# Kernel tuning notes

Hardware: AMD Instinct MI355X
Metric: run time of the kernel (lower is better)

Reference implementation:

```python
import jax, jax.numpy as jnp
import numpy as np

L = 4        # num decoder layers
H = 8        # heads
D = 512      # d_model
DFF = 2048   # ffn hidden
V = 8000     # target vocab
B = 16       # batch
S_ENC = 128  # encoder seq len
T = 32       # decode target_length
START, END, NULL = 1, 2, 0
NEG = -1e9
EPS = 1e-6


def sinusoid_pos(max_len, d):
    pos = np.arange(max_len)[:, None].astype(np.float32)
    i = np.arange(d)[None, :].astype(np.float32)
    ang = pos / np.power(10000.0, (2.0 * np.floor(i / 2.0)) / d)
    pe = np.where(np.arange(d)[None, :] % 2 == 0, np.sin(ang), np.cos(ang))
    return jnp.asarray(pe[None], jnp.float32)  # [1, max_len, d]


def setup_inputs() -> dict:
    key = jax.random.key(0)
    ks = jax.random.split(key, 16)
    g = lambda k, shape: jax.random.normal(k, shape, jnp.float32) * 0.02
    return {
        "target_length": T,
        "encoder_output": jax.random.normal(ks[0], (B, S_ENC, D), jnp.float32),
        "padding_mask": jnp.zeros((B, S_ENC), jnp.float32),  # 1.0 where padded
        "embed": g(ks[1], (V, D)),
        "wq": g(ks[2], (L, D, D)), "wk": g(ks[3], (L, D, D)),
        "wv": g(ks[4], (L, D, D)), "wo": g(ks[5], (L, D, D)),
        "cwq": g(ks[6], (L, D, D)), "cwk": g(ks[7], (L, D, D)),
        "cwv": g(ks[8], (L, D, D)), "cwo": g(ks[9], (L, D, D)),
        "w1": g(ks[10], (L, D, DFF)), "b1": jnp.zeros((L, DFF), jnp.float32),
        "w2": g(ks[11], (L, DFF, D)), "b2": jnp.zeros((L, D), jnp.float32),
        "ln_g": jnp.ones((L, 3, D), jnp.float32), "ln_b": jnp.zeros((L, 3, D), jnp.float32),
        "fc_w": g(ks[12], (D, V)), "fc_b": jnp.zeros((V,), jnp.float32),
    }


def ln(x, g, b):
    m = jnp.mean(x, axis=-1, keepdims=True)
    v = jnp.mean(jnp.square(x - m), axis=-1, keepdims=True)
    return (x - m) * jax.lax.rsqrt(v + EPS) * g + b


def mha(q_in, kv_in, wq, wk, wv, wo, mask):
    Bn, Sq, d = q_in.shape
    dh = d // H
    q = (q_in @ wq).reshape(Bn, Sq, H, dh)
    k = (kv_in @ wk).reshape(Bn, -1, H, dh)
    v = (kv_in @ wv).reshape(Bn, -1, H, dh)
    s = jnp.einsum('bqhd,bkhd->bhqk', q, k) / jnp.sqrt(jnp.float32(dh)) + mask
    a = jax.nn.softmax(s, axis=-1)
    o = jnp.einsum('bhqk,bkhd->bqhd', a, v).reshape(Bn, Sq, d)
    return o @ wo


def decoder_stack(x, encoder_output, self_mask, cross_mask,
                  wq, wk, wv, wo, cwq, cwk, cwv, cwo,
                  w1, b1, w2, b2, ln_g, ln_b):
    for i in range(L):
        a = mha(x, x, wq[i], wk[i], wv[i], wo[i], self_mask)
        x = ln(x + a, ln_g[i, 0], ln_b[i, 0])
        a2 = mha(x, encoder_output, cwq[i], cwk[i], cwv[i], cwo[i], cross_mask)
        x = ln(x + a2, ln_g[i, 1], ln_b[i, 1])
        f = jax.nn.relu(x @ w1[i] + b1[i]) @ w2[i] + b2[i]
        x = ln(x + f, ln_g[i, 2], ln_b[i, 2])
    return x


def reference(target_length, encoder_output, padding_mask, embed,
              wq, wk, wv, wo, cwq, cwk, cwv, cwo,
              w1, b1, w2, b2, ln_g, ln_b, fc_w, fc_b):
    Bn, S, d = encoder_output.shape
    Tp1 = target_length + 1
    pos_enc = sinusoid_pos(Tp1, d)
    sqrt_d = jnp.sqrt(jnp.float32(d))
    cross_mask = padding_mask[:, None, None, :] * NEG  # [B,1,1,S_enc]
    tokens0 = jnp.full((Bn, Tp1), NULL, jnp.int32).at[:, 0].set(START)
    done0 = jnp.zeros((Bn,), bool)

    def step(carry, t):
        tokens, done = carry
        # re-embed the whole (fixed-size, masked) prefix buffer each step
        x = embed[tokens] * sqrt_d + pos_enc
        # only positions <= t are valid keys; no look-ahead mask (matches original)
        self_mask = jnp.where(jnp.arange(Tp1) <= t, 0.0, NEG)[None, None, None, :]
        x = decoder_stack(x, encoder_output, self_mask, cross_mask,
                          wq, wk, wv, wo, cwq, cwk, cwv, cwo,
                          w1, b1, w2, b2, ln_g, ln_b)
        out = x[:, t, :] @ fc_w + fc_b  # logits at last valid position
        max_idx = jnp.argmax(out, axis=-1).astype(jnp.int32)
        done = done | (max_idx == END)
        tok = jnp.where(done, jnp.int32(NULL), max_idx)
        tokens = tokens.at[:, t + 1].set(tok)
        return (tokens, done), None

    (tokens, done), _ = jax.lax.scan(step, (tokens0, done0), jnp.arange(target_length))
    return tokens[:, 1:].astype(jnp.int64)
```

## Files before the change

kernel.cpp:

```cpp
#include <hip/hip_runtime.h>
#include <math.h>

#define L_   4
#define H_   8
#define D_   512
#define DH   64
#define DFF_ 2048
#define V_   8000
#define B_   16
#define SENC 128
#define T_   32
#define TP1  33
#define NEGV -1e9f
#define EPSV 1e-6f
#define SQRTD 22.627416997969522f
#define XSZ  ((size_t)TP1 * B_ * D_)

__global__ __launch_bounds__(256) void gemm32_k(
    const float* __restrict__ A, const float* __restrict__ W,
    const float* __restrict__ bias, float* __restrict__ C,
    int M, int N, int K, int kchunk, size_t pstride, int relu, int tmode)
{
    __shared__ __align__(16) float As[2][16][34];
    __shared__ __align__(16) float Bs[2][16][68];
    int tid = threadIdx.x;
    int tx = tid & 15, ty = tid >> 4;
    int m0 = blockIdx.y * 32, n0 = blockIdx.x * 64;
    int kbeg = blockIdx.z * kchunk;
    int niter = kchunk >> 4;
    C += (size_t)blockIdx.z * pstride;
    int am = tid >> 2, aseg = tid & 3;
    int bk = tid >> 4, bc4 = (tid & 15) * 4;
    float4 aReg = make_float4(0.f, 0.f, 0.f, 0.f), bReg;
    {
        int k0 = kbeg;
        if (tid < 128) {
            int gm = m0 + am;
            if (gm < M) aReg = *(const float4*)&A[(size_t)gm * K + k0 + aseg * 4];
        }
        bReg = *(const float4*)&W[(size_t)(k0 + bk) * N + n0 + bc4];
    }
    if (tid < 128) {
        As[0][aseg * 4 + 0][am] = aReg.x;
        As[0][aseg * 4 + 1][am] = aReg.y;
        As[0][aseg * 4 + 2][am] = aReg.z;
        As[0][aseg * 4 + 3][am] = aReg.w;
    }
    *(float4*)&Bs[0][bk][bc4] = bReg;
    __syncthreads();
    float acc[2][4] = {};
    for (int it = 0; it < niter; it++) {
        int cur = it & 1;
        if (it + 1 < niter) {
            int k0 = kbeg + (it + 1) * 16;
            if (tid < 128) {
                int gm = m0 + am;
                aReg = make_float4(0.f, 0.f, 0.f, 0.f);
                if (gm < M) aReg = *(const float4*)&A[(size_t)gm * K + k0 + aseg * 4];
            }
            bReg = *(const float4*)&W[(size_t)(k0 + bk) * N + n0 + bc4];
        }
        #pragma unroll
        for (int kk = 0; kk < 16; kk++) {
            float2 a2 = *(const float2*)&As[cur][kk][ty * 2];
            float4 b4 = *(const float4*)&Bs[cur][kk][tx * 4];
            acc[0][0] += a2.x * b4.x; acc[0][1] += a2.x * b4.y;
            acc[0][2] += a2.x * b4.z; acc[0][3] += a2.x * b4.w;
            acc[1][0] += a2.y * b4.x; acc[1][1] += a2.y * b4.y;
            acc[1][2] += a2.y * b4.z; acc[1][3] += a2.y * b4.w;
        }
        if (it + 1 < niter) {
            int nxt = 1 - cur;
            if (tid < 128) {
                As[nxt][aseg * 4 + 0][am] = aReg.x;
                As[nxt][aseg * 4 + 1][am] = aReg.y;
                As[nxt][aseg * 4 + 2][am] = aReg.z;
                As[nxt][aseg * 4 + 3][am] = aReg.w;
            }
            *(float4*)&Bs[nxt][bk][bc4] = bReg;
        }
        __syncthreads();
    }
    #pragma unroll
    for (int i = 0; i < 2; i++) {
        int gm = m0 + ty * 2 + i;
        if (gm >= M) continue;
        #pragma unroll
        for (int j = 0; j < 4; j++) {
            int gn = n0 + tx * 4 + j;
            float vv = acc[i][j];
            if (bias) vv += bias[gn];
            if (relu) vv = fmaxf(vv, 0.f);
            if (tmode == 1)
                C[(size_t)(gm >> 7) * 65536 + (size_t)gn * SENC + (gm & 127)] = vv;
            else
                C[(size_t)gm * N + gn] = vv;
        }
    }
}

__global__ __launch_bounds__(256) void gemm_qkv_k(
    const float* __restrict__ A, const float* __restrict__ W0,
    const float* __restrict__ W1, const float* __restrict__ W2,
    float* __restrict__ Cb, int M)
{
    __shared__ __align__(16) float As[2][16][34];
    __shared__ __align__(16) float Bs[2][16][68];
    int sel = blockIdx.x >> 3;
    const float* W = (sel == 0) ? W0 : ((sel == 1) ? W1 : W2);
    float* C = Cb + (size_t)sel * XSZ;
    int tid = threadIdx.x;
    int tx = tid & 15, ty = tid >> 4;
    int m0 = blockIdx.y * 32, n0 = (blockIdx.x & 7) * 64;
    int am = tid >> 2, aseg = tid & 3;
    int bk = tid >> 4, bc4 = (tid & 15) * 4;
    float4 aReg = make_float4(0.f, 0.f, 0.f, 0.f), bReg;
    {
        if (tid < 128) {
            int gm = m0 + am;
            if (gm < M) aReg = *(const float4*)&A[(size_t)gm * D_ + aseg * 4];
        }
        bReg = *(const float4*)&W[(size_t)bk * D_ + n0 + bc4];
    }
    if (tid < 128) {
        As[0][aseg * 4 + 0][am] = aReg.x;
        As[0][aseg * 4 + 1][am] = aReg.y;
        As[0][aseg * 4 + 2][am] = aReg.z;
        As[0][aseg * 4 + 3][am] = aReg.w;
    }
    *(float4*)&Bs[0][bk][bc4] = bReg;
    __syncthreads();
    float acc[2][4] = {};
    for (int it = 0; it < 32; it++) {
        int cur = it & 1;
        if (it + 1 < 32) {
            int k0 = (it + 1) * 16;
            if (tid < 128) {
                int gm = m0 + am;
                aReg = make_float4(0.f, 0.f, 0.f, 0.f);
                if (gm < M) aReg = *(const float4*)&A[(size_t)gm * D_ + k0 + aseg * 4];
            }
            bReg = *(const float4*)&W[(size_t)(k0 + bk) * D_ + n0 + bc4];
        }
        #pragma unroll
        for (int kk = 0; kk < 16; kk++) {
            float2 a2 = *(const float2*)&As[cur][kk][ty * 2];
            float4 b4 = *(const float4*)&Bs[cur][kk][tx * 4];
            acc[0][0] += a2.x * b4.x; acc[0][1] += a2.x * b4.y;
            acc[0][2] += a2.x * b4.z; acc[0][3] += a2.x * b4.w;
            acc[1][0] += a2.y * b4.x; acc[1][1] += a2.y * b4.y;
            acc[1][2] += a2.y * b4.z; acc[1][3] += a2.y * b4.w;
        }
        if (it + 1 < 32) {
            int nxt = 1 - cur;
            if (tid < 128) {
                As[nxt][aseg * 4 + 0][am] = aReg.x;
                As[nxt][aseg * 4 + 1][am] = aReg.y;
                As[nxt][aseg * 4 + 2][am] = aReg.z;
                As[nxt][aseg * 4 + 3][am] = aReg.w;
            }
            *(float4*)&Bs[nxt][bk][bc4] = bReg;
        }
        __syncthreads();
    }
    #pragma unroll
    for (int i = 0; i < 2; i++) {
        int gm = m0 + ty * 2 + i;
        if (gm >= M) continue;
        #pragma unroll
        for (int j = 0; j < 4; j++) {
            int gn = n0 + tx * 4 + j;
            if (sel == 1)
                C[(size_t)(gm & 15) * 16896 + (size_t)gn * TP1 + (gm >> 4)] =
                    acc[i][j];
            else
                C[(size_t)gm * D_ + gn] = acc[i][j];
        }
    }
}

__global__ void init_k(int* __restrict__ tokens, int* __restrict__ done,
                       float* __restrict__ cmask, const float* __restrict__ pm)
{
    int tid = threadIdx.x + blockIdx.x * 256;
    if (tid < B_ * TP1) tokens[tid] = ((tid % TP1) == 0) ? 1 : 0;
    if (tid < B_) done[tid] = 0;
    if (tid < B_ * SENC) cmask[tid] = pm[tid] * NEGV;
}

__global__ __launch_bounds__(256) void embed_k(
    const float* __restrict__ embed, const int* __restrict__ tokens,
    float* __restrict__ x)
{
    int p = blockIdx.x;
    int b = blockIdx.y;
    int tok = tokens[b * TP1 + p];
    const float* e = embed + (size_t)tok * D_;
    float* xr = x + ((size_t)p * B_ + b) * D_;
    for (int d = threadIdx.x; d < D_; d += 256) {
        float fd = (float)(2 * (d / 2)) / (float)D_;
        float ang = (float)p / powf(10000.f, fd);
        float pe = (d & 1) ? cosf(ang) : sinf(ang);
        xr[d] = e[d] * SQRTD + pe;
    }
}

__device__ __forceinline__ float block_sum(float s) {
    __shared__ float red[4];
    #pragma unroll
    for (int off = 32; off; off >>= 1) s += __shfl_xor(s, off);
    if ((threadIdx.x & 63) == 0) red[threadIdx.x >> 6] = s;
    __syncthreads();
    float tot = red[0] + red[1] + red[2] + red[3];
    __syncthreads();
    return tot;
}

__global__ __launch_bounds__(256) void attn_mega_k(
    const float* __restrict__ q, const float* __restrict__ kT,
    const float* __restrict__ v, const float* __restrict__ wo,
    const float* __restrict__ KcT, const float* __restrict__ Vc,
    const float* __restrict__ cmask, const float* __restrict__ cwq,
    const float* __restrict__ cwo, float* __restrict__ x,
    const float* __restrict__ lg, const float* __restrict__ lb, int P)
{
    int r = blockIdx.x, b = r & 15;
    int tid = threadIdx.x;
    int c0 = tid * 2;
    __shared__ float xs[D_], arow[D_];
    __shared__ float scs[H_][SENC];
    __shared__ float inv[H_];
    {
        int kp = tid & 31, h = tid >> 5;
        float acc = 0.f;
        if (kp < P) {
            const float* qr = q + (size_t)r * D_ + h * 64;
            const float* kb = kT + ((size_t)(b * 8 + h) * 64) * TP1 + kp;
            #pragma unroll 8
            for (int d = 0; d < 64; d++) acc += qr[d] * kb[(size_t)d * TP1];
        }
        scs[h][kp] = acc * 0.125f;
    }
    __syncthreads();
    if (tid < 8) {
        float mx = -1e30f;
        for (int j = 0; j < P; j++) mx = fmaxf(mx, scs[tid][j]);
        float sum = 0.f;
        for (int j = 0; j < P; j++) {
            float e = expf(scs[tid][j] - mx);
            scs[tid][j] = e;
            sum += e;
        }
        inv[tid] = 1.f / sum;
    }
    __syncthreads();
    {
        int h = c0 >> 6;
        float o0 = 0.f, o1 = 0.f;
        for (int j = 0; j < P; j++) {
            float2 vv = *(const float2*)&v[((size_t)j * B_ + b) * D_ + c0];
            float w = scs[h][j];
            o0 += w * vv.x; o1 += w * vv.y;
        }
        arow[c0]     = o0 * inv[h];
        arow[c0 + 1] = o1 * inv[h];
    }
    __syncthreads();
    {
        float2 xv = *(const float2*)&x[(size_t)r * D_ + c0];
        float v0 = xv.x, v1 = xv.y;
        #pragma unroll 8
        for (int k = 0; k < D_; k++) {
            float a = arow[k];
            float2 wv = *(const float2*)&wo[(size_t)k * D_ + c0];
            v0 += a * wv.x; v1 += a * wv.y;
        }
        float mean = block_sum(v0 + v1) * (1.f / 512.f);
        float d0 = v0 - mean, d1 = v1 - mean;
        float var = block_sum(d0 * d0 + d1 * d1) * (1.f / 512.f);
        float rs = rsqrtf(var + EPSV);
        xs[c0]     = d0 * rs * lg[c0]     + lb[c0];
        xs[c0 + 1] = d1 * rs * lg[c0 + 1] + lb[c0 + 1];
    }
    __syncthreads();
    {
        float q0 = 0.f, q1 = 0.f;
        #pragma unroll 8
        for (int k = 0; k < D_; k++) {
            float a = xs[k];
            float2 wv = *(const float2*)&cwq[(size_t)k * D_ + c0];
            q0 += a * wv.x; q1 += a * wv.y;
        }
        arow[c0] = q0; arow[c0 + 1] = q1;
    }
    __syncthreads();
    #pragma unroll
    for (int j = 0; j < 4; j++) {
        int idx = tid + j * 256;
        int h = idx >> 7, s = idx & 127;
        const float* kb = KcT + ((size_t)(b * 512 + h * 64)) * SENC + s;
        float acc = 0.f;
        #pragma unroll 8
        for (int d = 0; d < 64; d++) acc += arow[h * 64 + d] * kb[(size_t)d * SENC];
        scs[h][s] = acc * 0.125f + cmask[b * SENC + s];
    }
    __syncthreads();
    if (tid < 8) {
        float mx = -1e30f;
        for (int s = 0; s < SENC; s++) mx = fmaxf(mx, scs[tid][s]);
        float sum = 0.f;
        for (int s = 0; s < SENC; s++) {
            float e = expf(scs[tid][s] - mx);
            scs[tid][s] = e;
            sum += e;
        }
        inv[tid] = 1.f / sum;
    }
    __syncthreads();
    {
        int h = c0 >> 6;
        float o0 = 0.f, o1 = 0.f;
        for (int s = 0; s < SENC; s++) {
            float2 vv = *(const float2*)&Vc[((size_t)b * SENC + s) * D_ + c0];
            float w = scs[h][s];
            o0 += w * vv.x; o1 += w * vv.y;
        }
        arow[c0]     = o0 * inv[h];
        arow[c0 + 1] = o1 * inv[h];
    }
    __syncthreads();
    {
        float v0 = xs[c0], v1 = xs[c0 + 1];
        #pragma unroll 8
        for (int k = 0; k < D_; k++) {
            float a = arow[k];
            float2 wv = *(const float2*)&cwo[(size_t)k * D_ + c0];
            v0 += a * wv.x; v1 += a * wv.y;
        }
        float mean = block_sum(v0 + v1) * (1.f / 512.f);
        float d0 = v0 - mean, d1 = v1 - mean;
        float var = block_sum(d0 * d0 + d1 * d1) * (1.f / 512.f);
        float rs = rsqrtf(var + EPSV);
        x[(size_t)r * D_ + c0]     = d0 * rs * lg[D_ + c0]     + lb[D_ + c0];
        x[(size_t)r * D_ + c0 + 1] = d1 * rs * lg[D_ + c0 + 1] + lb[D_ + c0 + 1];
    }
}

__global__ __launch_bounds__(256) void ln_red_k(
    float* __restrict__ x, const float* __restrict__ parts, size_t pstride,
    int nparts, const float* __restrict__ bias,
    const float* __restrict__ gam, const float* __restrict__ bet)
{
    int r = blockIdx.x;
    float* xr = x + (size_t)r * D_;
    int tid = threadIdx.x;
    float v0 = xr[tid];
    float v1 = xr[tid + 256];
    for (int s = 0; s < nparts; s++) {
        const float* pr = parts + (size_t)s * pstride + (size_t)r * D_;
        v0 += pr[tid];
        v1 += pr[tid + 256];
    }
    if (bias) { v0 += bias[tid]; v1 += bias[tid + 256]; }
    float mean = block_sum(v0 + v1) * (1.f / 512.f);
    float d0 = v0 - mean, d1 = v1 - mean;
    float var = block_sum(d0 * d0 + d1 * d1) * (1.f / 512.f);
    float rs = rsqrtf(var + EPSV);
    xr[tid]       = d0 * rs * gam[tid] + bet[tid];
    xr[tid + 256] = d1 * rs * gam[tid + 256] + bet[tid + 256];
}

__global__ __launch_bounds__(256) void logits_k(
    const float* __restrict__ x, const float* __restrict__ fcw,
    const float* __restrict__ fcb, float* __restrict__ cand_v,
    int* __restrict__ cand_i, int t)
{
    __shared__ float xs[B_][D_];
    __shared__ float red[4][64][B_];
    int tid = threadIdx.x;
    for (int i = tid; i < B_ * D_; i += 256) {
        int b = i >> 9, d = i & 511;
        xs[b][d] = x[((size_t)t * B_ + b) * D_ + d];
    }
    __syncthreads();
    int lane = tid & 63, ks = tid >> 6;
    int col = blockIdx.x * 64 + lane;
    float acc[B_] = {};
    int kb = ks * 128;
    for (int k = kb; k < kb + 128; k++) {
        float w = fcw[(size_t)k * V_ + col];
        #pragma unroll
        for (int b = 0; b < B_; b++) acc[b] += xs[b][k] * w;
    }
    #pragma unroll
    for (int b = 0; b < B_; b++) red[ks][lane][b] = acc[b];
    __syncthreads();
    if (ks == 0) {
        float bias = fcb[col];
        #pragma unroll
        for (int b = 0; b < B_; b++) {
            float val = red[0][lane][b] + red[1][lane][b]
                      + red[2][lane][b] + red[3][lane][b] + bias;
            int idx = col;
            #pragma unroll
            for (int off = 32; off; off >>= 1) {
                float ov = __shfl_down(val, off);
                int oi = __shfl_down(idx, off);
                if (ov > val || (ov == val && oi < idx)) { val = ov; idx = oi; }
            }
            if (lane == 0) {
                cand_v[(size_t)b * 125 + blockIdx.x] = val;
                cand_i[(size_t)b * 125 + blockIdx.x] = idx;
            }
        }
    }
}

__global__ __launch_bounds__(128) void argmax_k(
    const float* __restrict__ cand_v, const int* __restrict__ cand_i,
    int* __restrict__ tokens, int* __restrict__ done, int t)
{
    int b = blockIdx.x;
    int tid = threadIdx.x;
    float val = -1e30f; int idx = 0x7fffffff;
    if (tid < 125) { val = cand_v[(size_t)b * 125 + tid]; idx = cand_i[(size_t)b * 125 + tid]; }
    __shared__ float sv[128];
    __shared__ int si[128];
    sv[tid] = val; si[tid] = idx;
    __syncthreads();
    for (int s = 64; s; s >>= 1) {
        if (tid < s) {
            float ov = sv[tid + s]; int oi = si[tid + s];
            if (ov > sv[tid] || (ov == sv[tid] && oi < si[tid])) {
                sv[tid] = ov; si[tid] = oi;
            }
        }
        __syncthreads();
    }
    if (tid == 0) {
        int best = si[0];
        int dn = done[b] | (best == 2 ? 1 : 0);
        done[b] = dn;
        tokens[b * TP1 + t + 1] = dn ? 0 : best;
    }
}

__global__ void writeout_k(const int* __restrict__ tokens, int* __restrict__ out)
{
    int i = threadIdx.x + blockIdx.x * 256;
    if (i < B_ * T_) {
        int b = i / T_, j = i % T_;
        out[i] = tokens[b * TP1 + j + 1];
    }
}

extern "C" void kernel_launch(void* const* d_in, const int* in_sizes, int n_in,
                              void* d_out, int out_size, void* d_ws, size_t ws_size,
                              hipStream_t stream)
{
    const float* enc   = (const float*)d_in[1];
    const float* pm    = (const float*)d_in[2];
    const float* embed = (const float*)d_in[3];
    const float* wq    = (const float*)d_in[4];
    const float* wk    = (const float*)d_in[5];
    const float* wv    = (const float*)d_in[6];
    const float* wo    = (const float*)d_in[7];
    const float* cwq   = (const float*)d_in[8];
    const float* cwk   = (const float*)d_in[9];
    const float* cwv   = (const float*)d_in[10];
    const float* cwo   = (const float*)d_in[11];
    const float* w1    = (const float*)d_in[12];
    const float* b1    = (const float*)d_in[13];
    const float* w2    = (const float*)d_in[14];
    const float* b2    = (const float*)d_in[15];
    const float* ln_g  = (const float*)d_in[16];
    const float* ln_b  = (const float*)d_in[17];
    const float* fcw   = (const float*)d_in[18];
    const float* fcb   = (const float*)d_in[19];

    float* ws = (float*)d_ws;
    size_t off = 0;
    float* x     = ws + off; off += XSZ;
    float* qkv   = ws + off; off += 3 * XSZ;
    float* parts = ws + off; off += 4 * XSZ;
    float* ffnh  = ws + off; off += (size_t)TP1 * B_ * DFF_;
    float* cand_v= ws + off; off += (size_t)B_ * 125;
    float* KcT   = ws + off; off += (size_t)L_ * B_ * SENC * D_;
    float* Vc    = ws + off; off += (size_t)L_ * B_ * SENC * D_;
    float* cmask = ws + off; off += (size_t)B_ * SENC;
    int* cand_i  = (int*)(ws + off); off += (size_t)B_ * 125;
    int* tokens  = (int*)(ws + off); off += (B_ * TP1 + 63) & ~63;
    int* done    = (int*)(ws + off); off += 64;

    init_k<<<8, 256, 0, stream>>>(tokens, done, cmask, pm);

    const size_t KVL = (size_t)B_ * SENC * D_;
    for (int l = 0; l < L_; l++) {
        gemm32_k<<<dim3(8, (B_ * SENC) / 32), 256, 0, stream>>>(
            enc, cwk + (size_t)l * D_ * D_, nullptr, KcT + l * KVL,
            B_ * SENC, D_, D_, D_, 0, 0, 1);
        gemm32_k<<<dim3(8, (B_ * SENC) / 32), 256, 0, stream>>>(
            enc, cwv + (size_t)l * D_ * D_, nullptr, Vc + l * KVL,
            B_ * SENC, D_, D_, D_, 0, 0, 0);
    }

    for (int t = 0; t < T_; t++) {
        int P = t + 1;
        int M = P * B_;
        int mt = (M + 31) / 32;

        embed_k<<<dim3(P, B_), 256, 0, stream>>>(embed, tokens, x);

        for (int l = 0; l < L_; l++) {
            const size_t lw = (size_t)l * D_ * D_;
            gemm_qkv_k<<<dim3(24, mt), 256, 0, stream>>>(
                x, wq + lw, wk + lw, wv + lw, qkv, M);
            attn_mega_k<<<M, 256, 0, stream>>>(
                qkv, qkv + XSZ, qkv + 2 * XSZ, wo + lw,
                KcT + l * KVL, Vc + l * KVL, cmask, cwq + lw, cwo + lw, x,
                ln_g + (size_t)(l * 3 + 0) * D_, ln_b + (size_t)(l * 3 + 0) * D_, P);
            gemm32_k<<<dim3(32, mt), 256, 0, stream>>>(
                x, w1 + (size_t)l * D_ * DFF_, b1 + (size_t)l * DFF_, ffnh,
                M, DFF_, D_, D_, 0, 1, 0);
            gemm32_k<<<dim3(8, mt, 4), 256, 0, stream>>>(
                ffnh, w2 + (size_t)l * DFF_ * D_, nullptr, parts,
                M, D_, DFF_, 512, XSZ, 0, 0);
            ln_red_k<<<M, 256, 0, stream>>>(x, parts, XSZ, 4, b2 + (size_t)l * D_,
                ln_g + (size_t)(l * 3 + 2) * D_, ln_b + (size_t)(l * 3 + 2) * D_);
        }

        logits_k<<<V_ / 64, 256, 0, stream>>>(x, fcw, fcb, cand_v, cand_i, t);
        argmax_k<<<B_, 128, 0, stream>>>(cand_v, cand_i, tokens, done, t);
    }

    writeout_k<<<2, 256, 0, stream>>>(tokens, (int*)d_out);
}
```

Measured before the change: 24.32 ms.

## Replace per-step kernel launches with a single persistent kernel using grid barriers

Folds all per-step kernels (embedding, QKV GEMM, attention, FFN, logits, argmax, writeout) into one persistent kernel of 256 blocks that steps through work lists and synchronises with an atomic-counter grid barrier. Embeddings of earlier tokens are cached in a separate buffer so each step only embeds the new token, and attention handles four query rows per block. The goal is to remove the launch overhead of hundreds of small kernels across 32 decode steps. The costs are spin-wait barriers, lower per-phase occupancy, and deadlock risk if all 256 blocks are not co-resident.

Measured after the change: 41.23 ms. 1.7x slower.

```diff
diff --git a/kernel.cpp b/kernel.cpp
--- a/kernel.cpp
+++ b/kernel.cpp
@@ -15,31 +15,63 @@
 #define EPSV 1e-6f
 #define SQRTD 22.627416997969522f
 #define XSZ  ((size_t)TP1 * B_ * D_)
-
-__global__ __launch_bounds__(256) void gemm32_k(
+#define KVL  ((size_t)B_ * SENC * D_)
+#define G_   256
+
+struct Prm {
+    const float *enc, *pm, *embed, *wq, *wk, *wv, *wo, *cwq, *cwk, *cwv, *cwo,
+                *w1, *b1, *w2, *b2, *ln_g, *ln_b, *fcw, *fcb;
+    float *x, *xemb, *qkv, *parts, *ffnh, *cand_v, *KcT, *Vc, *cmask;
+    int *cand_i, *tokens, *done, *bar, *outp;
+};
+
+union SMem {
+    struct { float As[2][16][34]; float Bs[2][16][68]; } g;
+    struct { float qa[4][D_]; float xs[4][D_]; float scs[4][H_][SENC];
+             float inv[4][H_]; } a;
+    struct { float xs[B_][D_]; float red[4][64][B_]; } lg;
+    struct { float sv[128]; int si[128]; } am;
+};
+
+__device__ __forceinline__ void gsync(int* cnt, int& epoch) {
+    __syncthreads();
+    if (threadIdx.x == 0) {
+        __threadfence();
+        epoch++;
+        atomicAdd(cnt, 1);
+        while (atomicAdd(cnt, 0) < epoch * G_)
+            __builtin_amdgcn_s_sleep(8);
+        __threadfence();
+    }
+    __syncthreads();
+}
+
+__device__ __forceinline__ float block_sum(float s, float* red) {
+    #pragma unroll
+    for (int off = 32; off; off >>= 1) s += __shfl_xor(s, off);
+    if ((threadIdx.x & 63) == 0) red[threadIdx.x >> 6] = s;
+    __syncthreads();
+    float tot = red[0] + red[1] + red[2] + red[3];
+    __syncthreads();
+    return tot;
+}
+
+__device__ void gemm_tile(float As[2][16][34], float Bs[2][16][68],
     const float* __restrict__ A, const float* __restrict__ W,
     const float* __restrict__ bias, float* __restrict__ C,
-    int M, int N, int K, int kchunk, size_t pstride, int relu, int tmode)
+    int M, int N, int K, int m0, int n0, int kbeg, int niter,
+    int relu, int tmode)
 {
-    __shared__ __align__(16) float As[2][16][34];
-    __shared__ __align__(16) float Bs[2][16][68];
     int tid = threadIdx.x;
     int tx = tid & 15, ty = tid >> 4;
-    int m0 = blockIdx.y * 32, n0 = blockIdx.x * 64;
-    int kbeg = blockIdx.z * kchunk;
-    int niter = kchunk >> 4;
-    C += (size_t)blockIdx.z * pstride;
     int am = tid >> 2, aseg = tid & 3;
     int bk = tid >> 4, bc4 = (tid & 15) * 4;
     float4 aReg = make_float4(0.f, 0.f, 0.f, 0.f), bReg;
-    {
-        int k0 = kbeg;
-        if (tid < 128) {
-            int gm = m0 + am;
-            if (gm < M) aReg = *(const float4*)&A[(size_t)gm * K + k0 + aseg * 4];
-        }
-        bReg = *(const float4*)&W[(size_t)(k0 + bk) * N + n0 + bc4];
-    }
+    if (tid < 128) {
+        int gm = m0 + am;
+        if (gm < M) aReg = *(const float4*)&A[(size_t)gm * K + kbeg + aseg * 4];
+    }
+    bReg = *(const float4*)&W[(size_t)(kbeg + bk) * N + n0 + bc4];
     if (tid < 128) {
         As[0][aseg * 4 + 0][am] = aReg.x;
         As[0][aseg * 4 + 1][am] = aReg.y;
@@ -91,366 +123,432 @@
             float vv = acc[i][j];
             if (bias) vv += bias[gn];
             if (relu) vv = fmaxf(vv, 0.f);
-            if (tmode == 1)
+            if (tmode == 0)
+                C[(size_t)gm * N + gn] = vv;
+            else if (tmode == 1)
                 C[(size_t)(gm >> 7) * 65536 + (size_t)gn * SENC + (gm & 127)] = vv;
             else
-                C[(size_t)gm * N + gn] = vv;
+                C[(size_t)(gm & 15) * 16896 + (size_t)gn * TP1 + (gm >> 4)] = vv;
         }
     }
 }
 
-__global__ __launch_bounds__(256) void gemm_qkv_k(
-    const float* __restrict__ A, const float* __restrict__ W0,
-    const float* __restrict__ W1, const float* __restrict__ W2,
-    float* __restrict__ Cb, int M)
+__global__ __launch_bounds__(256) void decoder_k(Prm p)
 {
-    __shared__ __align__(16) float As[2][16][34];
-    __shared__ __align__(16) float Bs[2][16][68];
-    int sel = blockIdx.x >> 3;
-    const float* W = (sel == 0) ? W0 : ((sel == 1) ? W1 : W2);
-    float* C = Cb + (size_t)sel * XSZ;
-    int tid = threadIdx.x;
-    int tx = tid & 15, ty = tid >> 4;
-    int m0 = blockIdx.y * 32, n0 = (blockIdx.x & 7) * 64;
-    int am = tid >> 2, aseg = tid & 3;
-    int bk = tid >> 4, bc4 = (tid & 15) * 4;
-    float4 aReg = make_float4(0.f, 0.f, 0.f, 0.f), bReg;
-    {
+    extern __shared__ char smem_raw[];
+    SMem& sm = *(SMem*)smem_raw;
+    __shared__ float bsred[4];
+    int bid = blockIdx.x, tid = threadIdx.x;
+    int c0 = tid * 2;
+    int epoch = 0;
+
+    if (bid == 0) {
+        for (int i = tid; i < B_ * TP1; i += 256)
+            p.tokens[i] = ((i % TP1) == 0) ? 1 : 0;
+        if (tid < B_) p.done[tid] = 0;
+    }
+    if (bid == 1) {
+        for (int i = tid; i < B_ * SENC; i += 256)
+            p.cmask[i] = p.pm[i] * NEGV;
+    }
+    gsync(p.bar, epoch);
+
+    for (int job = bid; job < L_ * 1024; job += G_) {
+        int l = job >> 10;
+        int w = job & 1;
+        int jn = (job >> 1) & 7;
+        int mr = (job >> 4) & 63;
+        gemm_tile(sm.g.As, sm.g.Bs, p.enc,
+                  (w ? p.cwv : p.cwk) + (size_t)l * D_ * D_, nullptr,
+                  (w ? p.Vc : p.KcT) + (size_t)l * KVL,
+                  B_ * SENC, D_, D_, mr * 32, jn * 64, 0, 32, 0, w ? 0 : 1);
+    }
+    gsync(p.bar, epoch);
+
+    for (int t = 0; t < T_; t++) {
+        int P = t + 1;
+        int M = P * B_;
+        int mt = (M + 31) / 32;
+
+        for (int job = bid; job < B_; job += G_) {
+            int b = job;
+            if (t > 0) {
+                if (tid < 128) {
+                    sm.am.sv[tid] = (tid < 125) ? p.cand_v[(size_t)b * 125 + tid] : -1e30f;
+                    sm.am.si[tid] = (tid < 125) ? p.cand_i[(size_t)b * 125 + tid] : 0x7fffffff;
+                }
+                __syncthreads();
+                for (int s = 64; s; s >>= 1) {
+                    if (tid < s) {
+                        float ov = sm.am.sv[tid + s]; int oi = sm.am.si[tid + s];
+                        if (ov > sm.am.sv[tid] ||
+                            (ov == sm.am.sv[tid] && oi < sm.am.si[tid])) {
+                            sm.am.sv[tid] = ov; sm.am.si[tid] = oi;
+                        }
+                    }
+                    __syncthreads();
+                }
+                if (tid == 0) {
+                    int idx = sm.am.si[0];
+                    int dn = p.done[b] | (idx == 2 ? 1 : 0);
+                    p.done[b] = dn;
+                    int tok = dn ? 0 : idx;
+                    p.tokens[b * TP1 + t] = tok;
+                    sm.am.si[0] = tok;
+                }
+                __syncthreads();
+            } else {
+                if (tid == 0) sm.am.si[0] = 1;
+                __syncthreads();
+            }
+            int tok = sm.am.si[0];
+            const float* e = p.embed + (size_t)tok * D_;
+            float* xr = p.xemb + ((size_t)t * B_ + b) * D_;
+            #pragma unroll
+            for (int u = 0; u < 2; u++) {
+                int c = c0 + u;
+                float fd = (float)(2 * (c / 2)) / (float)D_;
+                float ang = (float)t / powf(10000.f, fd);
+                float pe = (c & 1) ? cosf(ang) : sinf(ang);
+                xr[c] = e[c] * SQRTD + pe;
+            }
+            __syncthreads();
+        }
+        gsync(p.bar, epoch);
+
+        for (int l = 0; l < L_; l++) {
+            const size_t lw = (size_t)l * D_ * D_;
+            const float* lgam = p.ln_g + (size_t)l * 3 * D_;
+            const float* lbet = p.ln_b + (size_t)l * 3 * D_;
+
+            const float* Aq = (l == 0) ? p.xemb : p.x;
+            int jmod = (l == 0) ? 25 : 24;
+            int nq = jmod * mt;
+            for (int job = bid; job < nq; job += G_) {
+                int jn = job % jmod;
+                int mr = job / jmod;
+                if (jn < 24) {
+                    int sel = jn >> 3;
+                    const float* W = (sel == 0) ? p.wq + lw
+                                   : (sel == 1) ? p.wk + lw : p.wv + lw;
+                    gemm_tile(sm.g.As, sm.g.Bs, Aq, W, nullptr,
+                              p.qkv + (size_t)sel * XSZ, M, D_, D_,
+                              mr * 32, (jn & 7) * 64, 0, 32, 0,
+                              sel == 1 ? 2 : 0);
+                } else {
+                    for (int i = tid; i < 32 * 128; i += 256) {
+                        int rr = mr * 32 + (i >> 7);
+                        if (rr < M)
+                            *(float4*)&p.x[(size_t)rr * D_ + (i & 127) * 4] =
+                                *(const float4*)&p.xemb[(size_t)rr * D_ + (i & 127) * 4];
+                    }
+                }
+            }
+            gsync(p.bar, epoch);
+
+            int ng = ((P + 3) >> 2) * B_;
+            for (int job = bid; job < ng; job += G_) {
+                int b = job & 15;
+                int g4 = job >> 4;
+                int prow[4];
+                #pragma unroll
+                for (int rr = 0; rr < 4; rr++) {
+                    int pp = 4 * g4 + rr;
+                    prow[rr] = (pp < P ? pp : P - 1) * B_ + b;
+                }
+                int nr = P - 4 * g4; if (nr > 4) nr = 4;
+                for (int i = tid; i < 4 * 256; i += 256) {
+                    int rr = i >> 8, cc = (i & 255) * 2;
+                    *(float2*)&sm.a.qa[rr][cc] =
+                        *(const float2*)&p.qkv[(size_t)prow[rr] * D_ + cc];
+                }
+                __syncthreads();
+                {
+                    int kp = tid & 31, h = tid >> 5;
+                    float acc[4] = {};
+                    if (kp < P) {
+                        const float* kb = p.qkv + XSZ +
+                            ((size_t)(b * 8 + h) * 64) * TP1 + kp;
+                        for (int d = 0; d < 64; d++) {
+                            float kv = kb[(size_t)d * TP1];
+                            #pragma unroll
+                            for (int rr = 0; rr < 4; rr++)
+                                acc[rr] += sm.a.qa[rr][h * 64 + d] * kv;
+                        }
+                    }
+                    #pragma unroll
+                    for (int rr = 0; rr < 4; rr++)
+                        sm.a.scs[rr][h][kp] = acc[rr] * 0.125f;
+                }
+                __syncthreads();
+                if (tid < 32) {
+                    int rr = tid >> 3, h = tid & 7;
+                    float mx = -1e30f;
+                    for (int j = 0; j < P; j++) mx = fmaxf(mx, sm.a.scs[rr][h][j]);
+                    float sum = 0.f;
+                    for (int j = 0; j < P; j++) {
+                        float e = expf(sm.a.scs[rr][h][j] - mx);
+                        sm.a.scs[rr][h][j] = e;
+                        sum += e;
+                    }
+                    sm.a.inv[rr][h] = 1.f / sum;
+                }
+                __syncthreads();
+                {
+                    int h = c0 >> 6;
+                    float o0[4] = {}, o1[4] = {};
+                    for (int j = 0; j < P; j++) {
+                        float2 vv = *(const float2*)&p.qkv[2 * XSZ +
+                            ((size_t)j * B_ + b) * D_ + c0];
+                        #pragma unroll
+                        for (int rr = 0; rr < 4; rr++) {
+                            float w = sm.a.scs[rr][h][j];
+                            o0[rr] += w * vv.x; o1[rr] += w * vv.y;
+                        }
+                    }
+                    __syncthreads();
+                    #pragma unroll
+                    for (int rr = 0; rr < 4; rr++) {
+                        float iv = sm.a.inv[rr][h];
+                        sm.a.qa[rr][c0] = o0[rr] * iv;
+                        sm.a.qa[rr][c0 + 1] = o1[rr] * iv;
+                    }
+                }
+                __syncthreads();
+                {
+                    float v0[4], v1[4];
+                    #pragma unroll
+                    for (int rr = 0; rr < 4; rr++) {
+                        float2 xv = *(const float2*)&p.x[(size_t)prow[rr] * D_ + c0];
+                        v0[rr] = xv.x; v1[rr] = xv.y;
+                    }
+                    for (int k = 0; k < D_; k++) {
+                        float2 wv = *(const float2*)&p.wo[lw + (size_t)k * D_ + c0];
+                        #pragma unroll
+                        for (int rr = 0; rr < 4; rr++) {
+                            float a = sm.a.qa[rr][k];
+                            v0[rr] += a * wv.x; v1[rr] += a * wv.y;
+                        }
+                    }
+                    for (int rr = 0; rr < 4; rr++) {
+                        float mean = block_sum(v0[rr] + v1[rr], bsred) * (1.f / 512.f);
+                        float d0 = v0[rr] - mean, d1 = v1[rr] - mean;
+                        float var = block_sum(d0 * d0 + d1 * d1, bsred) * (1.f / 512.f);
+                        float rs = rsqrtf(var + EPSV);
+                        sm.a.xs[rr][c0]     = d0 * rs * lgam[c0]     + lbet[c0];
+                        sm.a.xs[rr][c0 + 1] = d1 * rs * lgam[c0 + 1] + lbet[c0 + 1];
+                    }
+                }
+                __syncthreads();
+                {
+                    float q0[4] = {}, q1[4] = {};
+                    for (int k = 0; k < D_; k++) {
+                        float2 wv = *(const float2*)&p.cwq[lw + (size_t)k * D_ + c0];
+                        #pragma unroll
+                        for (int rr = 0; rr < 4; rr++) {
+                            float a = sm.a.xs[rr][k];
+                            q0[rr] += a * wv.x; q1[rr] += a * wv.y;
+                        }
+                    }
+                    __syncthreads();
+                    #pragma unroll
+                    for (int rr = 0; rr < 4; rr++) {
+                        sm.a.qa[rr][c0] = q0[rr];
+                        sm.a.qa[rr][c0 + 1] = q1[rr];
+                    }
+                }
+                __syncthreads();
+                #pragma unroll
+                for (int jj = 0; jj < 4; jj++) {
+                    int idx = tid + jj * 256;
+                    int h = idx >> 7, s = idx & 127;
+                    const float* kb = p.KcT + (size_t)l * KVL +
+                        ((size_t)(b * 8 + h) * 64) * SENC + s;
+                    float acc[4] = {};
+                    for (int d = 0; d < 64; d++) {
+                        float kv = kb[(size_t)d * SENC];
+                        #pragma unroll
+                        for (int rr = 0; rr < 4; rr++)
+                            acc[rr] += sm.a.qa[rr][h * 64 + d] * kv;
+                    }
+                    float cm = p.cmask[b * SENC + s];
+                    #pragma unroll
+                    for (int rr = 0; rr < 4; rr++)
+                        sm.a.scs[rr][h][s] = acc[rr] * 0.125f + cm;
+                }
+                __syncthreads();
+                if (tid < 32) {
+                    int rr = tid >> 3, h = tid & 7;
+                    float mx = -1e30f;
+                    for (int s = 0; s < SENC; s++) mx = fmaxf(mx, sm.a.scs[rr][h][s]);
+                    float sum = 0.f;
+                    for (int s = 0; s < SENC; s++) {
+                        float e = expf(sm.a.scs[rr][h][s] - mx);
+                        sm.a.scs[rr][h][s] = e;
+                        sum += e;
+                    }
+                    sm.a.inv[rr][h] = 1.f / sum;
+                }
+                __syncthreads();
+                {
+                    int h = c0 >> 6;
+                    float o0[4] = {}, o1[4] = {};
+                    for (int s = 0; s < SENC; s++) {
+                        float2 vv = *(const float2*)&p.Vc[(size_t)l * KVL +
+                            ((size_t)b * SENC + s) * D_ + c0];
+                        #pragma unroll
+                        for (int rr = 0; rr < 4; rr++) {
+                            float w = sm.a.scs[rr][h][s];
+                            o0[rr] += w * vv.x; o1[rr] += w * vv.y;
+                        }
+                    }
+                    __syncthreads();
+                    #pragma unroll
+                    for (int rr = 0; rr < 4; rr++) {
+                        float iv = sm.a.inv[rr][h];
+                        sm.a.qa[rr][c0] = o0[rr] * iv;
+                        sm.a.qa[rr][c0 + 1] = o1[rr] * iv;
+                    }
+                }
+                __syncthreads();
+                {
+                    float v0[4], v1[4];
+                    #pragma unroll
+                    for (int rr = 0; rr < 4; rr++) {
+                        v0[rr] = sm.a.xs[rr][c0]; v1[rr] = sm.a.xs[rr][c0 + 1];
+                    }
+                    for (int k = 0; k < D_; k++) {
+                        float2 wv = *(const float2*)&p.cwo[lw + (size_t)k * D_ + c0];
+                        #pragma unroll
+                        for (int rr = 0; rr < 4; rr++) {
+                            float a = sm.a.qa[rr][k];
+                            v0[rr] += a * wv.x; v1[rr] += a * wv.y;
+                        }
+                    }
+                    for (int rr = 0; rr < 4; rr++) {
+                        float mean = block_sum(v0[rr] + v1[rr], bsred) * (1.f / 512.f);
+                        float d0 = v0[rr] - mean, d1 = v1[rr] - mean;
+                        float var = block_sum(d0 * d0 + d1 * d1, bsred) * (1.f / 512.f);
+                        float rs = rsqrtf(var + EPSV);
+                        if (rr < nr) {
+                            p.x[(size_t)prow[rr] * D_ + c0] =
+                                d0 * rs * lgam[D_ + c0] + lbet[D_ + c0];
+                            p.x[(size_t)prow[rr] * D_ + c0 + 1] =
+                                d1 * rs * lgam[D_ + c0 + 1] + lbet[D_ + c0 + 1];
+                        }
+                    }
+                }
+                __syncthreads();
+            }
+            gsync(p.bar, epoch);
+
+            for (int job = bid; job < 32 * mt; job += G_) {
+                int jn = job & 31, mr = job >> 5;
+                gemm_tile(sm.g.As, sm.g.Bs, p.x,
+                          p.w1 + (size_t)l * D_ * DFF_, p.b1 + (size_t)l * DFF_,
+                          p.ffnh, M, DFF_, D_, mr * 32, jn * 64, 0, 32, 1, 0);
+            }
+            gsync(p.bar, epoch);
+
+            for (int job = bid; job < 32 * mt; job += G_) {
+                int kz = job & 3, jn = (job >> 2) & 7, mr = job >> 5;
+                gemm_tile(sm.g.As, sm.g.Bs, p.ffnh,
+                          p.w2 + (size_t)l * DFF_ * D_, nullptr,
+                          p.parts + (size_t)kz * XSZ, M, D_, DFF_,
+                          mr * 32, jn * 64, kz * 512, 32, 0, 0);
+            }
+            gsync(p.bar, epoch);
+
+            for (int job = bid; job < M; job += G_) {
+                float* xr = p.x + (size_t)job * D_;
+                float v0 = xr[tid], v1 = xr[tid + 256];
+                for (int s = 0; s < 4; s++) {
+                    const float* pr = p.parts + (size_t)s * XSZ + (size_t)job * D_;
+                    v0 += pr[tid]; v1 += pr[tid + 256];
+                }
+                v0 += p.b2[(size_t)l * D_ + tid];
+                v1 += p.b2[(size_t)l * D_ + tid + 256];
+                float mean = block_sum(v0 + v1, bsred) * (1.f / 512.f);
+                float d0 = v0 - mean, d1 = v1 - mean;
+                float var = block_sum(d0 * d0 + d1 * d1, bsred) * (1.f / 512.f);
+                float rs = rsqrtf(var + EPSV);
+                xr[tid]       = d0 * rs * lgam[2 * D_ + tid]       + lbet[2 * D_ + tid];
+                xr[tid + 256] = d1 * rs * lgam[2 * D_ + tid + 256] + lbet[2 * D_ + tid + 256];
+                __syncthreads();
+            }
+            gsync(p.bar, epoch);
+        }
+
+        for (int job = bid; job < 125; job += G_) {
+            for (int i = tid; i < B_ * D_; i += 256) {
+                int b = i >> 9, d = i & 511;
+                sm.lg.xs[b][d] = p.x[((size_t)t * B_ + b) * D_ + d];
+            }
+            __syncthreads();
+            int lane = tid & 63, ks = tid >> 6;
+            int col = job * 64 + lane;
+            float acc[B_] = {};
+            int kb = ks * 128;
+            for (int k = kb; k < kb + 128; k++) {
+                float w = p.fcw[(size_t)k * V_ + col];
+                #pragma unroll
+                for (int b = 0; b < B_; b++) acc[b] += sm.lg.xs[b][k] * w;
+            }
+            #pragma unroll
+            for (int b = 0; b < B_; b++) sm.lg.red[ks][lane][b] = acc[b];
+            __syncthreads();
+            if (ks == 0) {
+                float bias = p.fcb[col];
+                #pragma unroll
+                for (int b = 0; b < B_; b++) {
+                    float val = sm.lg.red[0][lane][b] + sm.lg.red[1][lane][b]
+                              + sm.lg.red[2][lane][b] + sm.lg.red[3][lane][b] + bias;
+                    int idx = col;
+                    #pragma unroll
+                    for (int off = 32; off; off >>= 1) {
+                        float ov = __shfl_down(val, off);
+                        int oi = __shfl_down(idx, off);
+                        if (ov > val || (ov == val && oi < idx)) { val = ov; idx = oi; }
+                    }
+                    if (lane == 0) {
+                        p.cand_v[(size_t)b * 125 + job] = val;
+                        p.cand_i[(size_t)b * 125 + job] = idx;
+                    }
+                }
+            }
+            __syncthreads();
+        }
+        gsync(p.bar, epoch);
+    }
+
+    for (int job = bid; job < B_; job += G_) {
+        int b = job;
         if (tid < 128) {
-            int gm = m0 + am;
-            if (gm < M) aReg = *(const float4*)&A[(size_t)gm * D_ + aseg * 4];
-        }
-        bReg = *(const float4*)&W[(size_t)bk * D_ + n0 + bc4];
-    }
-    if (tid < 128) {
-        As[0][aseg * 4 + 0][am] = aReg.x;
-        As[0][aseg * 4 + 1][am] = aReg.y;
-        As[0][aseg * 4 + 2][am] = aReg.z;
-        As[0][aseg * 4 + 3][am] = aReg.w;
-    }
-    *(float4*)&Bs[0][bk][bc4] = bReg;
-    __syncthreads();
-    float acc[2][4] = {};
-    for (int it = 0; it < 32; it++) {
-        int cur = it & 1;
-        if (it + 1 < 32) {
-            int k0 = (it + 1) * 16;
-            if (tid < 128) {
-                int gm = m0 + am;
-                aReg = make_float4(0.f, 0.f, 0.f, 0.f);
-                if (gm < M) aReg = *(const float4*)&A[(size_t)gm * D_ + k0 + aseg * 4];
-            }
-            bReg = *(const float4*)&W[(size_t)(k0 + bk) * D_ + n0 + bc4];
-        }
-        #pragma unroll
-        for (int kk = 0; kk < 16; kk++) {
-            float2 a2 = *(const float2*)&As[cur][kk][ty * 2];
-            float4 b4 = *(const float4*)&Bs[cur][kk][tx * 4];
-            acc[0][0] += a2.x * b4.x; acc[0][1] += a2.x * b4.y;
-            acc[0][2] += a2.x * b4.z; acc[0][3] += a2.x * b4.w;
-            acc[1][0] += a2.y * b4.x; acc[1][1] += a2.y * b4.y;
-            acc[1][2] += a2.y * b4.z; acc[1][3] += a2.y * b4.w;
-        }
-        if (it + 1 < 32) {
-            int nxt = 1 - cur;
-            if (tid < 128) {
-                As[nxt][aseg * 4 + 0][am] = aReg.x;
-                As[nxt][aseg * 4 + 1][am] = aReg.y;
-                As[nxt][aseg * 4 + 2][am] = aReg.z;
-                As[nxt][aseg * 4 + 3][am] = aReg.w;
-            }
-            *(float4*)&Bs[nxt][bk][bc4] = bReg;
+            sm.am.sv[tid] = (tid < 125) ? p.cand_v[(size_t)b * 125 + tid] : -1e30f;
+            sm.am.si[tid] = (tid < 125) ? p.cand_i[(size_t)b * 125 + tid] : 0x7fffffff;
         }
         __syncthreads();
-    }
-    #pragma unroll
-    for (int i = 0; i < 2; i++) {
-        int gm = m0 + ty * 2 + i;
-        if (gm >= M) continue;
-        #pragma unroll
-        for (int j = 0; j < 4; j++) {
-            int gn = n0 + tx * 4 + j;
-            if (sel == 1)
-                C[(size_t)(gm & 15) * 16896 + (size_t)gn * TP1 + (gm >> 4)] =
-                    acc[i][j];
-            else
-                C[(size_t)gm * D_ + gn] = acc[i][j];
-        }
-    }
-}
-
-__global__ void init_k(int* __restrict__ tokens, int* __restrict__ done,
-                       float* __restrict__ cmask, const float* __restrict__ pm)
-{
-    int tid = threadIdx.x + blockIdx.x * 256;
-    if (tid < B_ * TP1) tokens[tid] = ((tid % TP1) == 0) ? 1 : 0;
-    if (tid < B_) done[tid] = 0;
-    if (tid < B_ * SENC) cmask[tid] = pm[tid] * NEGV;
-}
-
-__global__ __launch_bounds__(256) void embed_k(
-    const float* __restrict__ embed, const int* __restrict__ tokens,
-    float* __restrict__ x)
-{
-    int p = blockIdx.x;
-    int b = blockIdx.y;
-    int tok = tokens[b * TP1 + p];
-    const float* e = embed + (size_t)tok * D_;
-    float* xr = x + ((size_t)p * B_ + b) * D_;
-    for (int d = threadIdx.x; d < D_; d += 256) {
-        float fd = (float)(2 * (d / 2)) / (float)D_;
-        float ang = (float)p / powf(10000.f, fd);
-        float pe = (d & 1) ? cosf(ang) : sinf(ang);
-        xr[d] = e[d] * SQRTD + pe;
-    }
-}
-
-__device__ __forceinline__ float block_sum(float s) {
-    __shared__ float red[4];
-    #pragma unroll
-    for (int off = 32; off; off >>= 1) s += __shfl_xor(s, off);
-    if ((threadIdx.x & 63) == 0) red[threadIdx.x >> 6] = s;
-    __syncthreads();
-    float tot = red[0] + red[1] + red[2] + red[3];
-    __syncthreads();
-    return tot;
-}
-
-__global__ __launch_bounds__(256) void attn_mega_k(
-    const float* __restrict__ q, const float* __restrict__ kT,
-    const float* __restrict__ v, const float* __restrict__ wo,
-    const float* __restrict__ KcT, const float* __restrict__ Vc,
-    const float* __restrict__ cmask, const float* __restrict__ cwq,
-    const float* __restrict__ cwo, float* __restrict__ x,
-    const float* __restrict__ lg, const float* __restrict__ lb, int P)
-{
-    int r = blockIdx.x, b = r & 15;
-    int tid = threadIdx.x;
-    int c0 = tid * 2;
-    __shared__ float xs[D_], arow[D_];
-    __shared__ float scs[H_][SENC];
-    __shared__ float inv[H_];
-    {
-        int kp = tid & 31, h = tid >> 5;
-        float acc = 0.f;
-        if (kp < P) {
-            const float* qr = q + (size_t)r * D_ + h * 64;
-            const float* kb = kT + ((size_t)(b * 8 + h) * 64) * TP1 + kp;
-            #pragma unroll 8
-            for (int d = 0; d < 64; d++) acc += qr[d] * kb[(size_t)d * TP1];
-        }
-        scs[h][kp] = acc * 0.125f;
-    }
-    __syncthreads();
-    if (tid < 8) {
-        float mx = -1e30f;
-        for (int j = 0; j < P; j++) mx = fmaxf(mx, scs[tid][j]);
-        float sum = 0.f;
-        for (int j = 0; j < P; j++) {
-            float e = expf(scs[tid][j] - mx);
-            scs[tid][j] = e;
-            sum += e;
-        }
-        inv[tid] = 1.f / sum;
-    }
-    __syncthreads();
-    {
-        int h = c0 >> 6;
-        float o0 = 0.f, o1 = 0.f;
-        for (int j = 0; j < P; j++) {
-            float2 vv = *(const float2*)&v[((size_t)j * B_ + b) * D_ + c0];
-            float w = scs[h][j];
-            o0 += w * vv.x; o1 += w * vv.y;
-        }
-        arow[c0]     = o0 * inv[h];
-        arow[c0 + 1] = o1 * inv[h];
-    }
-    __syncthreads();
-    {
-        float2 xv = *(const float2*)&x[(size_t)r * D_ + c0];
-        float v0 = xv.x, v1 = xv.y;
-        #pragma unroll 8
-        for (int k = 0; k < D_; k++) {
-            float a = arow[k];
-            float2 wv = *(const float2*)&wo[(size_t)k * D_ + c0];
-            v0 += a * wv.x; v1 += a * wv.y;
-        }
-        float mean = block_sum(v0 + v1) * (1.f / 512.f);
-        float d0 = v0 - mean, d1 = v1 - mean;
-        float var = block_sum(d0 * d0 + d1 * d1) * (1.f / 512.f);
-        float rs = rsqrtf(var + EPSV);
-        xs[c0]     = d0 * rs * lg[c0]     + lb[c0];
-        xs[c0 + 1] = d1 * rs * lg[c0 + 1] + lb[c0 + 1];
-    }
-    __syncthreads();
-    {
-        float q0 = 0.f, q1 = 0.f;
-        #pragma unroll 8
-        for (int k = 0; k < D_; k++) {
-            float a = xs[k];
-            float2 wv = *(const float2*)&cwq[(size_t)k * D_ + c0];
-            q0 += a * wv.x; q1 += a * wv.y;
-        }
-        arow[c0] = q0; arow[c0 + 1] = q1;
-    }
-    __syncthreads();
-    #pragma unroll
-    for (int j = 0; j < 4; j++) {
-        int idx = tid + j * 256;
-        int h = idx >> 7, s = idx & 127;
-        const float* kb = KcT + ((size_t)(b * 512 + h * 64)) * SENC + s;
-        float acc = 0.f;
-        #pragma unroll 8
-        for (int d = 0; d < 64; d++) acc += arow[h * 64 + d] * kb[(size_t)d * SENC];
-        scs[h][s] = acc * 0.125f + cmask[b * SENC + s];
-    }
-    __syncthreads();
-    if (tid < 8) {
-        float mx = -1e30f;
-        for (int s = 0; s < SENC; s++) mx = fmaxf(mx, scs[tid][s]);
-        float sum = 0.f;
-        for (int s = 0; s < SENC; s++) {
-            float e = expf(scs[tid][s] - mx);
-            scs[tid][s] = e;
-            sum += e;
-        }
-        inv[tid] = 1.f / sum;
-    }
-    __syncthreads();
-    {
-        int h = c0 >> 6;
-        float o0 = 0.f, o1 = 0.f;
-        for (int s = 0; s < SENC; s++) {
-            float2 vv = *(const float2*)&Vc[((size_t)b * SENC + s) * D_ + c0];
-            float w = scs[h][s];
-            o0 += w * vv.x; o1 += w * vv.y;
-        }
-        arow[c0]     = o0 * inv[h];
-        arow[c0 + 1] = o1 * inv[h];
-    }
-    __syncthreads();
-    {
-        float v0 = xs[c0], v1 = xs[c0 + 1];
-        #pragma unroll 8
-        for (int k = 0; k < D_; k++) {
-            float a = arow[k];
-            float2 wv = *(const float2*)&cwo[(size_t)k * D_ + c0];
-            v0 += a * wv.x; v1 += a * wv.y;
-        }
-        float mean = block_sum(v0 + v1) * (1.f / 512.f);
-        float d0 = v0 - mean, d1 = v1 - mean;
-        float var = block_sum(d0 * d0 + d1 * d1) * (1.f / 512.f);
-        float rs = rsqrtf(var + EPSV);
-        x[(size_t)r * D_ + c0]     = d0 * rs * lg[D_ + c0]     + lb[D_ + c0];
-        x[(size_t)r * D_ + c0 + 1] = d1 * rs * lg[D_ + c0 + 1] + lb[D_ + c0 + 1];
-    }
-}
-
-__global__ __launch_bounds__(256) void ln_red_k(
-    float* __restrict__ x, const float* __restrict__ parts, size_t pstride,
-    int nparts, const float* __restrict__ bias,
-    const float* __restrict__ gam, const float* __restrict__ bet)
-{
-    int r = blockIdx.x;
-    float* xr = x + (size_t)r * D_;
-    int tid = threadIdx.x;
-    float v0 = xr[tid];
-    float v1 = xr[tid + 256];
-    for (int s = 0; s < nparts; s++) {
-        const float* pr = parts + (size_t)s * pstride + (size_t)r * D_;
-        v0 += pr[tid];
-        v1 += pr[tid + 256];
-    }
-    if (bias) { v0 += bias[tid]; v1 += bias[tid + 256]; }
-    float mean = block_sum(v0 + v1) * (1.f / 512.f);
-    float d0 = v0 - mean, d1 = v1 - mean;
-    float var = block_sum(d0 * d0 + d1 * d1) * (1.f / 512.f);
-    float rs = rsqrtf(var + EPSV);
-    xr[tid]       = d0 * rs * gam[tid] + bet[tid];
-    xr[tid + 256] = d1 * rs * gam[tid + 256] + bet[tid + 256];
-}
-
-__global__ __launch_bounds__(256) void logits_k(
-    const float* __restrict__ x, const float* __restrict__ fcw,
-    const float* __restrict__ fcb, float* __restrict__ cand_v,
-    int* __restrict__ cand_i, int t)
-{
-    __shared__ float xs[B_][D_];
-    __shared__ float red[4][64][B_];
-    int tid = threadIdx.x;
-    for (int i = tid; i < B_ * D_; i += 256) {
-        int b = i >> 9, d = i & 511;
-        xs[b][d] = x[((size_t)t * B_ + b) * D_ + d];
-    }
-    __syncthreads();
-    int lane = tid & 63, ks = tid >> 6;
-    int col = blockIdx.x * 64 + lane;
-    float acc[B_] = {};
-    int kb = ks * 128;
-    for (int k = kb; k < kb + 128; k++) {
-        float w = fcw[(size_t)k * V_ + col];
-        #pragma unroll
-        for (int b = 0; b < B_; b++) acc[b] += xs[b][k] * w;
-    }
-    #pragma unroll
-    for (int b = 0; b < B_; b++) red[ks][lane][b] = acc[b];
-    __syncthreads();
-    if (ks == 0) {
-        float bias = fcb[col];
-        #pragma unroll
-        for (int b = 0; b < B_; b++) {
-            float val = red[0][lane][b] + red[1][lane][b]
-                      + red[2][lane][b] + red[3][lane][b] + bias;
-            int idx = col;
-            #pragma unroll
-            for (int off = 32; off; off >>= 1) {
-                float ov = __shfl_down(val, off);
-                int oi = __shfl_down(idx, off);
-                if (ov > val || (ov == val && oi < idx)) { val = ov; idx = oi; }
-            }
-            if (lane == 0) {
-                cand_v[(size_t)b * 125 + blockIdx.x] = val;
-                cand_i[(size_t)b * 125 + blockIdx.x] = idx;
-            }
-        }
-    }
-}
-
-__global__ __launch_bounds__(128) void argmax_k(
-    const float* __restrict__ cand_v, const int* __restrict__ cand_i,
-    int* __restrict__ tokens, int* __restrict__ done, int t)
-{
-    int b = blockIdx.x;
-    int tid = threadIdx.x;
-    float val = -1e30f; int idx = 0x7fffffff;
-    if (tid < 125) { val = cand_v[(size_t)b * 125 + tid]; idx = cand_i[(size_t)b * 125 + tid]; }
-    __shared__ float sv[128];
-    __shared__ int si[128];
-    sv[tid] = val; si[tid] = idx;
-    __syncthreads();
-    for (int s = 64; s; s >>= 1) {
-        if (tid < s) {
-            float ov = sv[tid + s]; int oi = si[tid + s];
-            if (ov > sv[tid] || (ov == sv[tid] && oi < si[tid])) {
-                sv[tid] = ov; si[tid] = oi;
-            }
+        for (int s = 64; s; s >>= 1) {
+            if (tid < s) {
+                float ov = sm.am.sv[tid + s]; int oi = sm.am.si[tid + s];
+                if (ov > sm.am.sv[tid] ||
+                    (ov == sm.am.sv[tid] && oi < sm.am.si[tid])) {
+                    sm.am.sv[tid] = ov; sm.am.si[tid] = oi;
+                }
+            }
+            __syncthreads();
+        }
+        if (tid == 0) {
+            int idx = sm.am.si[0];
+            int dn = p.done[b] | (idx == 2 ? 1 : 0);
+            sm.am.si[0] = dn ? 0 : idx;
         }
         __syncthreads();
-    }
-    if (tid == 0) {
-        int best = si[0];
-        int dn = done[b] | (best == 2 ? 1 : 0);
-        done[b] = dn;
-        tokens[b * TP1 + t + 1] = dn ? 0 : best;
-    }
-}
-
-__global__ void writeout_k(const int* __restrict__ tokens, int* __restrict__ out)
-{
-    int i = threadIdx.x + blockIdx.x * 256;
-    if (i < B_ * T_) {
-        int b = i / T_, j = i % T_;
-        out[i] = tokens[b * TP1 + j + 1];
+        if (tid < T_) {
+            int v = (tid == T_ - 1) ? sm.am.si[0] : p.tokens[b * TP1 + tid + 1];
+            p.outp[b * T_ + tid] = v;
+        }
+        __syncthreads();
     }
 }
 
@@ -458,80 +556,48 @@
                               void* d_out, int out_size, void* d_ws, size_t ws_size,
                               hipStream_t stream)
 {
-    const float* enc   = (const float*)d_in[1];
-    const float* pm    = (const float*)d_in[2];
-    const float* embed = (const float*)d_in[3];
-    const float* wq    = (const float*)d_in[4];
-    const float* wk    = (const float*)d_in[5];
-    const float* wv    = (const float*)d_in[6];
-    const float* wo    = (const float*)d_in[7];
-    const float* cwq   = (const float*)d_in[8];
-    const float* cwk   = (const float*)d_in[9];
-    const float* cwv   = (const float*)d_in[10];
-    const float* cwo   = (const float*)d_in[11];
-    const float* w1    = (const float*)d_in[12];
-    const float* b1    = (const float*)d_in[13];
-    const float* w2    = (const float*)d_in[14];
-    const float* b2    = (const float*)d_in[15];
-    const float* ln_g  = (const float*)d_in[16];
-    const float* ln_b  = (const float*)d_in[17];
-    const float* fcw   = (const float*)d_in[18];
-    const float* fcb   = (const float*)d_in[19];
+    Prm p;
+    p.enc   = (const float*)d_in[1];
+    p.pm    = (const float*)d_in[2];
+    p.embed = (const float*)d_in[3];
+    p.wq    = (const float*)d_in[4];
+    p.wk    = (const float*)d_in[5];
+    p.wv    = (const float*)d_in[6];
+    p.wo    = (const float*)d_in[7];
+    p.cwq   = (const float*)d_in[8];
+    p.cwk   = (const float*)d_in[9];
+    p.cwv   = (const float*)d_in[10];
+    p.cwo   = (const float*)d_in[11];
+    p.w1    = (const float*)d_in[12];
+    p.b1    = (const float*)d_in[13];
+    p.w2    = (const float*)d_in[14];
+    p.b2    = (const float*)d_in[15];
+    p.ln_g  = (const float*)d_in[16];
+    p.ln_b  = (const float*)d_in[17];
+    p.fcw   = (const float*)d_in[18];
+    p.fcb   = (const float*)d_in[19];
 
     float* ws = (float*)d_ws;
     size_t off = 0;
-    float* x     = ws + off; off += XSZ;
-    float* qkv   = ws + off; off += 3 * XSZ;
-    float* parts = ws + off; off += 4 * XSZ;
-    float* ffnh  = ws + off; off += (size_t)TP1 * B_ * DFF_;
-    float* cand_v= ws + off; off += (size_t)B_ * 125;
-    float* KcT   = ws + off; off += (size_t)L_ * B_ * SENC * D_;
-    float* Vc    = ws + off; off += (size_t)L_ * B_ * SENC * D_;
-    float* cmask = ws + off; off += (size_t)B_ * SENC;
-    int* cand_i  = (int*)(ws + off); off += (size_t)B_ * 125;
-    int* tokens  = (int*)(ws + off); off += (B_ * TP1 + 63) & ~63;
-    int* done    = (int*)(ws + off); off += 64;
-
-    init_k<<<8, 256, 0, stream>>>(tokens, done, cmask, pm);
-
-    const size_t KVL = (size_t)B_ * SENC * D_;
-    for (int l = 0; l < L_; l++) {
-        gemm32_k<<<dim3(8, (B_ * SENC) / 32), 256, 0, stream>>>(
-            enc, cwk + (size_t)l * D_ * D_, nullptr, KcT + l * KVL,
-            B_ * SENC, D_, D_, D_, 0, 0, 1);
-        gemm32_k<<<dim3(8, (B_ * SENC) / 32), 256, 0, stream>>>(
-            enc, cwv + (size_t)l * D_ * D_, nullptr, Vc + l * KVL,
-            B_ * SENC, D_, D_, D_, 0, 0, 0);
-    }
-
-    for (int t = 0; t < T_; t++) {
-        int P = t + 1;
-        int M = P * B_;
-        int mt = (M + 31) / 32;
-
-        embed_k<<<dim3(P, B_), 256, 0, stream>>>(embed, tokens, x);
-
-        for (int l = 0; l < L_; l++) {
-            const size_t lw = (size_t)l * D_ * D_;
-            gemm_qkv_k<<<dim3(24, mt), 256, 0, stream>>>(
-                x, wq + lw, wk + lw, wv + lw, qkv, M);
-            attn_mega_k<<<M, 256, 0, stream>>>(
-                qkv, qkv + XSZ, qkv + 2 * XSZ, wo + lw,
-                KcT + l * KVL, Vc + l * KVL, cmask, cwq + lw, cwo + lw, x,
-                ln_g + (size_t)(l * 3 + 0) * D_, ln_b + (size_t)(l * 3 + 0) * D_, P);
-            gemm32_k<<<dim3(32, mt), 256, 0, stream>>>(
-                x, w1 + (size_t)l * D_ * DFF_, b1 + (size_t)l * DFF_, ffnh,
-                M, DFF_, D_, D_, 0, 1, 0);
-            gemm32_k<<<dim3(8, mt, 4), 256, 0, stream>>>(
-                ffnh, w2 + (size_t)l * DFF_ * D_, nullptr, parts,
-                M, D_, DFF_, 512, XSZ, 0, 0);
-            ln_red_k<<<M, 256, 0, stream>>>(x, parts, XSZ, 4, b2 + (size_t)l * D_,
-                ln_g + (size_t)(l * 3 + 2) * D_, ln_b + (size_t)(l * 3 + 2) * D_);
-        }
-
-        logits_k<<<V_ / 64, 256, 0, stream>>>(x, fcw, fcb, cand_v, cand_i, t);
-        argmax_k<<<B_, 128, 0, stream>>>(cand_v, cand_i, tokens, done, t);
-    }
-
-    writeout_k<<<2, 256, 0, stream>>>(tokens, (int*)d_out);
+    p.x      = ws + off; off += XSZ;
+    p.xemb   = ws + off; off += XSZ;
+    p.qkv    = ws + off; off += 3 * XSZ;
+    p.parts  = ws + off; off += 4 * XSZ;
+    p.ffnh   = ws + off; off += (size_t)TP1 * B_ * DFF_;
+    p.cand_v = ws + off; off += (size_t)B_ * 125;
+    p.KcT    = ws + off; off += (size_t)L_ * KVL;
+    p.Vc     = ws + off; off += (size_t)L_ * KVL;
+    p.cmask  = ws + off; off += (size_t)B_ * SENC;
+    p.cand_i = (int*)(ws + off); off += (size_t)B_ * 125;
+    p.tokens = (int*)(ws + off); off += (B_ * TP1 + 63) & ~63;
+    p.done   = (int*)(ws + off); off += 64;
+    p.bar    = (int*)(ws + off); off += 64;
+    p.outp   = (int*)d_out;
+
+    hipMemsetAsync(p.bar, 0, 256, stream);
+
+    const int smem_bytes = 86016;
+    hipFuncSetAttribute((const void*)decoder_k,
+                        hipFuncAttributeMaxDynamicSharedMemorySize, smem_bytes);
+    decoder_k<<<dim3(G_), dim3(256), smem_bytes, stream>>>(p);
 }
```
